# Optimization experiments

Measured on AMD Instinct MI355X. Metric: run time of the kernel, lower is better.

The kernel has to match this reference:

```python
import jax, jax.numpy as jnp
import numpy as np

WS = 7  # window_size


def setup_inputs() -> dict:
    key = jax.random.key(0)
    ks = jax.random.split(key, 4)
    B, C, H, W = 4, 384, 56, 56
    NH = 12
    x = jax.random.normal(ks[0], (B, C, H, W), dtype=jnp.float32)
    # 1x1 conv weights act as per-pixel linear maps over channels
    w_qkv = jax.random.normal(ks[1], (3 * C, C), dtype=jnp.float32) * (C ** -0.5)
    b_qkv = jnp.zeros((3 * C,), dtype=jnp.float32)
    w_proj = jax.random.normal(ks[2], (C, C), dtype=jnp.float32) * (C ** -0.5)
    b_proj = jnp.zeros((C,), dtype=jnp.float32)
    rel_bias = jax.random.normal(ks[3], (NH, WS, WS), dtype=jnp.float32) * 0.02
    return {"x": x, "w_qkv": w_qkv, "b_qkv": b_qkv,
            "w_proj": w_proj, "b_proj": b_proj, "rel_bias": rel_bias}


def reference(x, w_qkv, b_qkv, w_proj, b_proj, rel_bias):
    # Neighborhood attention: each query (i,j) attends to a ws x ws window of
    # keys/values centered at (i,j); borders handled by replication padding
    # (ReplicationPad2d), with a learned relative position bias (nh, ws, ws).
    B, C, H, W = x.shape
    nh, ws, _ = rel_bias.shape
    hd = C // nh
    p = ws // 2
    scale = hd ** -0.5

    # qkv 1x1 conv -> (B, 3, nh, hd, H, W)
    qkv = jnp.einsum('oc,bchw->bohw', w_qkv, x) + b_qkv[None, :, None, None]
    qkv = qkv.reshape(B, 3, nh, hd, H, W)
    q, k, v = qkv[:, 0] * scale, qkv[:, 1], qkv[:, 2]

    pad = ((0, 0), (0, 0), (0, 0), (p, p), (p, p))
    k_pad = jnp.pad(k, pad, mode='edge')  # replication padding
    v_pad = jnp.pad(v, pad, mode='edge')

    # attention logits over the ws*ws window offsets: (B, nh, H, W, K)
    logits = jnp.stack(
        [jnp.einsum('bnchw,bnchw->bnhw', q, k_pad[..., di:di + H, dj:dj + W])
         for di in range(ws) for dj in range(ws)], axis=-1)
    logits = logits + rel_bias.reshape(nh, ws * ws)[None, :, None, None, :]
    attn = jax.nn.softmax(logits, axis=-1)  # (attn_drop is identity in eval)

    # value windows: (B, nh, K, hd, H, W)
    v_win = jnp.stack([v_pad[..., di:di + H, dj:dj + W]
                       for di in range(ws) for dj in range(ws)], axis=2)
    out = jnp.einsum('bnhwk,bnkchw->bnchw', attn, v_win).reshape(B, C, H, W)

    # output projection 1x1 conv (proj_drop is identity in eval)
    out = jnp.einsum('oc,bchw->bohw', w_proj, out) + b_proj[None, :, None, None]
    return out
```

## Files before the change

kernel.cpp:

```cpp
#include <hip/hip_runtime.h>
#include <hip/hip_bf16.h>
#include <hip/hip_fp16.h>

#define S_HW 3136
#define SP   3200
#define IMG_W 56
#define C_DIM 384
#define NH_DIM 12
#define QKV_C 1152

#define TB 16
#define HALO 22
#define NPX 484
#define PLANE_B 3880

typedef float f32x4 __attribute__((ext_vector_type(4)));
typedef float f32x2 __attribute__((ext_vector_type(2)));
typedef short bf16x8 __attribute__((ext_vector_type(8)));
typedef _Float16 f16x2 __attribute__((ext_vector_type(2)));

__device__ __forceinline__ void gld_lds16(const void* g, void* lds) {
    __builtin_amdgcn_global_load_lds(
        (const __attribute__((address_space(1))) void*)g,
        (__attribute__((address_space(3))) void*)lds, 16, 0, 0);
}

__device__ __forceinline__ float u2f(unsigned int u) { return __uint_as_float(u); }
__device__ __forceinline__ unsigned int f2bf_bits(float f) {
    unsigned int u = __float_as_uint(f);
    u += 0x7FFF + ((u >> 16) & 1);
    return u >> 16;
}
__device__ __forceinline__ unsigned int f2h_bits(float f) {
    return (unsigned int)__half_as_ushort(__float2half(f));
}

__global__ __launch_bounds__(256) void convert_w2_kernel(
    const float* __restrict__ a, int na, __hip_bfloat16* __restrict__ oa,
    const float* __restrict__ b, int nb, __hip_bfloat16* __restrict__ ob)
{
    int i = blockIdx.x * 256 + threadIdx.x;
    if (i < na) oa[i] = __float2bfloat16(a[i]);
    else if (i < na + nb) ob[i - na] = __float2bfloat16(b[i - na]);
}

__global__ __launch_bounds__(256) void transpose_convert_kernel(
    const float* __restrict__ x, __hip_bfloat16* __restrict__ xt)
{
    __shared__ float t[32][33];
    const int b = blockIdx.z;
    const int c0 = blockIdx.y * 32, s0 = blockIdx.x * 32;
    const int tid = threadIdx.x;

    const int lc = tid >> 3, ls = (tid & 7) * 4;
    float4 v = *reinterpret_cast<const float4*>(
        &x[((size_t)b * C_DIM + c0 + lc) * S_HW + s0 + ls]);
    t[lc][ls + 0] = v.x; t[lc][ls + 1] = v.y;
    t[lc][ls + 2] = v.z; t[lc][ls + 3] = v.w;
    __syncthreads();

    const int ws = tid >> 3, wc = (tid & 7) * 4;
    uint2 pk;
    pk.x = f2bf_bits(t[wc + 0][ws]) | (f2bf_bits(t[wc + 1][ws]) << 16);
    pk.y = f2bf_bits(t[wc + 2][ws]) | (f2bf_bits(t[wc + 3][ws]) << 16);
    *reinterpret_cast<uint2*>(
        &xt[((size_t)b * SP + s0 + ws) * C_DIM + c0 + wc]) = pk;
}

template <bool TRANS_OUT, int NF, typename OutT>
__global__ __launch_bounds__(256) void gemm_bf16_mfma(
    const __hip_bfloat16* __restrict__ A,
    const __hip_bfloat16* __restrict__ Bt,
    const float* __restrict__ bias,
    OutT* __restrict__ Y,
    int O, int K, float qscale, int qrows)
{
    constexpr int BN = NF * 32;
    __shared__ char smem[8192 + BN * 64];
    char* As = smem;
    char* Bs = smem + 8192;

    const int b   = blockIdx.z;
    const int m0  = blockIdx.y * 128;
    const int n0  = blockIdx.x * BN;
    const int tid = threadIdx.x;
    const int w = tid >> 6, l = tid & 63;
    const int wr = w >> 1, wc = w & 1;

    const int srow = l >> 2;
    const int skk  = (l & 3) * 8;

    const __hip_bfloat16* Bb = Bt + (size_t)b * SP * K;

    f32x4 acc[4][NF];
    #pragma unroll
    for (int i = 0; i < 4; ++i)
        #pragma unroll
        for (int j = 0; j < NF; ++j) {
            f32x4 z = {0.f, 0.f, 0.f, 0.f};
            acc[i][j] = z;
        }

    const int frow = l & 15;
    const int fk   = (l >> 4) * 16;

    for (int k0 = 0; k0 < K; k0 += 32) {
        #pragma unroll
        for (int j = 0; j < 2; ++j) {
            const int chunk = w * 2 + j;
            const int m = chunk * 16 + srow;
            gld_lds16(A + (size_t)(m0 + m) * K + k0 + skk, As + chunk * 1024);
        }
        if (NF == 4) {
            #pragma unroll
            for (int j = 0; j < 2; ++j) {
                const int chunk = w * 2 + j;
                const int m = chunk * 16 + srow;
                gld_lds16(Bb + (size_t)(n0 + m) * K + k0 + skk, Bs + chunk * 1024);
            }
        } else {
            const int m = w * 16 + srow;
            gld_lds16(Bb + (size_t)(n0 + m) * K + k0 + skk, Bs + w * 1024);
        }
        __syncthreads();
        bf16x8 af[4], bfr[NF];
        #pragma unroll
        for (int mi = 0; mi < 4; ++mi)
            af[mi] = *reinterpret_cast<const bf16x8*>(
                As + (wr * 64 + mi * 16 + frow) * 64 + fk);
        #pragma unroll
        for (int ni = 0; ni < NF; ++ni)
            bfr[ni] = *reinterpret_cast<const bf16x8*>(
                Bs + (wc * (NF * 16) + ni * 16 + frow) * 64 + fk);
        #pragma unroll
        for (int mi = 0; mi < 4; ++mi)
            #pragma unroll
            for (int ni = 0; ni < NF; ++ni)
                acc[mi][ni] = __builtin_amdgcn_mfma_f32_16x16x32_bf16(
                    af[mi], bfr[ni], acc[mi][ni], 0, 0, 0);
        __syncthreads();
    }

    const int crow0 = (l >> 4) * 4;
    const int ccol  = l & 15;
    if (TRANS_OUT) {
        __hip_bfloat16* Yb = (__hip_bfloat16*)Y + (size_t)b * SP * O;
        #pragma unroll
        for (int ni = 0; ni < NF; ++ni) {
            const int col = n0 + wc * (NF * 16) + ni * 16 + ccol;
            if (col >= S_HW) continue;
            #pragma unroll
            for (int mi = 0; mi < 4; ++mi) {
                const int row0 = m0 + wr * 64 + mi * 16 + crow0;
                const float sc = (row0 < qrows) ? qscale : 1.f;
                float v0 = (acc[mi][ni][0] + bias[row0 + 0]) * sc;
                float v1 = (acc[mi][ni][1] + bias[row0 + 1]) * sc;
                float v2 = (acc[mi][ni][2] + bias[row0 + 2]) * sc;
                float v3 = (acc[mi][ni][3] + bias[row0 + 3]) * sc;
                uint2 pk;
                pk.x = f2h_bits(v0) | (f2h_bits(v1) << 16);
                pk.y = f2h_bits(v2) | (f2h_bits(v3) << 16);
                *reinterpret_cast<uint2*>(&Yb[(size_t)col * O + row0]) = pk;
            }
        }
    } else {
        float* Yb = (float*)Y + (size_t)b * O * S_HW;
        #pragma unroll
        for (int ni = 0; ni < NF; ++ni) {
            const int col = n0 + wc * (NF * 16) + ni * 16 + ccol;
            if (col >= S_HW) continue;
            #pragma unroll
            for (int mi = 0; mi < 4; ++mi) {
                #pragma unroll
                for (int r = 0; r < 4; ++r) {
                    const int row = m0 + wr * 64 + mi * 16 + crow0 + r;
                    float v = acc[mi][ni][r] + bias[row];
                    if (row < qrows) v *= qscale;
                    Yb[(size_t)row * S_HW + col] = v;
                }
            }
        }
    }
}

__global__ __launch_bounds__(256, 2) void na_attn_kernel(
    const __hip_bfloat16* __restrict__ qkvt, const float* __restrict__ rel_bias,
    __hip_bfloat16* __restrict__ outt)
{
    __shared__ alignas(16) char halo[8 * PLANE_B];

    const int blk  = blockIdx.x;
    const int tile = blk & 15;
    const int bn   = blk >> 4;
    const int nh   = bn % NH_DIM;
    const int b    = bn / NH_DIM;
    const int th0  = (tile >> 2) * TB;
    const int tw0  = (tile & 3) * TB;

    const int tid = threadIdx.x;
    const int ty = tid >> 4, tx = tid & 15;
    const int h = th0 + ty, w = tw0 + tx;
    const bool valid = (h < 56) && (w < 56);
    const int s = h * IMG_W + w;

    const __hip_bfloat16* base = qkvt + (size_t)b * SP * QKV_C;
    const int co = nh * 32;

    #pragma unroll
    for (int i = 0; i < 8; ++i) {
        const int idx = tid + i * 256;
        if (idx < NPX * 4) {
            const int px = idx >> 2, g = idx & 3;
            const int hy = px / HALO, hx = px - hy * HALO;
            const int y = min(max(th0 - 3 + hy, 0), 55);
            const int x = min(max(tw0 - 3 + hx, 0), 55);
            const uint4 v = *reinterpret_cast<const uint4*>(
                base + (size_t)(y * IMG_W + x) * QKV_C + C_DIM + co + g * 8);
            uint2 lo; lo.x = v.x; lo.y = v.y;
            uint2 hi; hi.x = v.z; hi.y = v.w;
            *reinterpret_cast<uint2*>(&halo[(2 * g + 0) * PLANE_B + px * 8]) = lo;
            *reinterpret_cast<uint2*>(&halo[(2 * g + 1) * PLANE_B + px * 8]) = hi;
        }
    }

    unsigned int qreg[16];
    if (valid) {
        const uint4* qp = reinterpret_cast<const uint4*>(base + (size_t)s * QKV_C + co);
        #pragma unroll
        for (int g = 0; g < 4; ++g) {
            uint4 qg = qp[g];
            qreg[4 * g + 0] = qg.x; qreg[4 * g + 1] = qg.y;
            qreg[4 * g + 2] = qg.z; qreg[4 * g + 3] = qg.w;
        }
    }
    __syncthreads();

    float logits[49];
    if (valid) {
        #pragma unroll
        for (int di = 0; di < 7; ++di) {
            #pragma unroll
            for (int dj = 0; dj < 7; ++dj) {
                const int hp = (ty + di) * HALO + (tx + dj);
                const char* hb = halo + hp * 8;
                float acc0 = 0.f, acc1 = 0.f;
                #pragma unroll
                for (int pl = 0; pl < 8; ++pl) {
                    uint2 kk = *reinterpret_cast<const uint2*>(hb + pl * PLANE_B);
#if __has_builtin(__builtin_amdgcn_fdot2)
                    acc0 = __builtin_amdgcn_fdot2(
                        __builtin_bit_cast(f16x2, qreg[2 * pl]),
                        __builtin_bit_cast(f16x2, kk.x), acc0, false);
                    acc1 = __builtin_amdgcn_fdot2(
                        __builtin_bit_cast(f16x2, qreg[2 * pl + 1]),
                        __builtin_bit_cast(f16x2, kk.y), acc1, false);
#else
                    f16x2 qa = __builtin_bit_cast(f16x2, qreg[2 * pl]);
                    f16x2 qb = __builtin_bit_cast(f16x2, qreg[2 * pl + 1]);
                    f16x2 ka = __builtin_bit_cast(f16x2, kk.x);
                    f16x2 kb = __builtin_bit_cast(f16x2, kk.y);
                    acc0 += (float)qa[0] * (float)ka[0] + (float)qa[1] * (float)ka[1];
                    acc1 += (float)qb[0] * (float)kb[0] + (float)qb[1] * (float)kb[1];
#endif
                }
                logits[di * 7 + dj] = acc0 + acc1 + rel_bias[(nh * 7 + di) * 7 + dj];
            }
        }
    }
    __syncthreads();

    #pragma unroll
    for (int i = 0; i < 8; ++i) {
        const int idx = tid + i * 256;
        if (idx < NPX * 4) {
            const int px = idx >> 2, g = idx & 3;
            const int hy = px / HALO, hx = px - hy * HALO;
            const int y = min(max(th0 - 3 + hy, 0), 55);
            const int x = min(max(tw0 - 3 + hx, 0), 55);
            const uint4 v = *reinterpret_cast<const uint4*>(
                base + (size_t)(y * IMG_W + x) * QKV_C + 2 * C_DIM + co + g * 8);
            uint2 lo; lo.x = v.x; lo.y = v.y;
            uint2 hi; hi.x = v.z; hi.y = v.w;
            *reinterpret_cast<uint2*>(&halo[(2 * g + 0) * PLANE_B + px * 8]) = lo;
            *reinterpret_cast<uint2*>(&halo[(2 * g + 1) * PLANE_B + px * 8]) = hi;
        }
    }

    unsigned int ppk[25];
    float inv = 0.f;
    if (valid) {
        float mx = logits[0];
        #pragma unroll
        for (int i = 1; i < 49; ++i) mx = fmaxf(mx, logits[i]);
        float sum = 0.f;
        #pragma unroll
        for (int i = 0; i < 24; ++i) {
            float e0 = __expf(logits[2 * i] - mx);
            float e1 = __expf(logits[2 * i + 1] - mx);
            sum += e0 + e1;
            ppk[i] = f2bf_bits(e0) << 16 | f2bf_bits(e1);
        }
        {
            float e0 = __expf(logits[48] - mx);
            sum += e0;
            ppk[24] = f2bf_bits(e0) << 16;
        }
        inv = 1.f / sum;
    }
    __syncthreads();

    if (valid) {
        float o[32];
        #pragma unroll
        for (int c = 0; c < 32; ++c) o[c] = 0.f;

        #pragma unroll
        for (int n = 0; n < 49; ++n) {
            const unsigned int pu = ppk[n >> 1];
            const float pv = (n & 1) ? u2f(pu << 16) : u2f(pu & 0xFFFF0000u);
            const int di = n / 7, dj = n % 7;
            const int hp = (ty + di) * HALO + (tx + dj);
            const char* hb = halo + hp * 8;
            #pragma unroll
            for (int pl = 0; pl < 8; ++pl) {
                uint2 vv = *reinterpret_cast<const uint2*>(hb + pl * PLANE_B);
                f16x2 va = __builtin_bit_cast(f16x2, vv.x);
                f16x2 vb = __builtin_bit_cast(f16x2, vv.y);
                o[4 * pl + 0] = fmaf((float)va[0], pv, o[4 * pl + 0]);
                o[4 * pl + 1] = fmaf((float)va[1], pv, o[4 * pl + 1]);
                o[4 * pl + 2] = fmaf((float)vb[0], pv, o[4 * pl + 2]);
                o[4 * pl + 3] = fmaf((float)vb[1], pv, o[4 * pl + 3]);
            }
        }

        uint4* dst = reinterpret_cast<uint4*>(outt + ((size_t)b * SP + s) * C_DIM + co);
        #pragma unroll
        for (int g = 0; g < 4; ++g) {
            uint4 pk;
            pk.x = f2bf_bits(o[8 * g + 0] * inv) | (f2bf_bits(o[8 * g + 1] * inv) << 16);
            pk.y = f2bf_bits(o[8 * g + 2] * inv) | (f2bf_bits(o[8 * g + 3] * inv) << 16);
            pk.z = f2bf_bits(o[8 * g + 4] * inv) | (f2bf_bits(o[8 * g + 5] * inv) << 16);
            pk.w = f2bf_bits(o[8 * g + 6] * inv) | (f2bf_bits(o[8 * g + 7] * inv) << 16);
            dst[g] = pk;
        }
    }
}

extern "C" void kernel_launch(void* const* d_in, const int* in_sizes, int n_in,
                              void* d_out, int out_size, void* d_ws, size_t ws_size,
                              hipStream_t stream) {
    const float* x        = (const float*)d_in[0];
    const float* w_qkv    = (const float*)d_in[1];
    const float* b_qkv    = (const float*)d_in[2];
    const float* w_proj   = (const float*)d_in[3];
    const float* b_proj   = (const float*)d_in[4];
    const float* rel_bias = (const float*)d_in[5];
    float* out = (float*)d_out;

    __hip_bfloat16* xt   = (__hip_bfloat16*)d_ws;
    __hip_bfloat16* wq   = xt + (size_t)4 * SP * C_DIM;
    __hip_bfloat16* wp   = wq + (size_t)QKV_C * C_DIM;
    __hip_bfloat16* qkvt = wp + (size_t)C_DIM * C_DIM;
    __hip_bfloat16* att  = qkvt + (size_t)4 * SP * QKV_C;

    const float scale = 0.17677669529663687f;
    const int nwq = QKV_C * C_DIM, nwp = C_DIM * C_DIM;

    convert_w2_kernel<<<dim3((nwq + nwp + 255) / 256), 256, 0, stream>>>(
        w_qkv, nwq, wq, w_proj, nwp, wp);
    transpose_convert_kernel<<<dim3(98, 12, 4), dim3(256), 0, stream>>>(x, xt);

    gemm_bf16_mfma<true, 4, __hip_bfloat16><<<dim3(25, 9, 4), 256, 0, stream>>>(
        wq, xt, b_qkv, qkvt, QKV_C, C_DIM, scale, C_DIM);

    na_attn_kernel<<<dim3(4 * NH_DIM * 16), 256, 0, stream>>>(qkvt, rel_bias, att);

    gemm_bf16_mfma<false, 2, float><<<dim3(50, 3, 4), 256, 0, stream>>>(
        wp, att, b_proj, out, C_DIM, C_DIM, 1.f, 0);
}
```

Before: 97.41 us.

## Split each attention pixel across two threads with DPP pair reduction

The neighborhood-attention kernel now uses 512 threads per block, with two adjacent lanes sharing one pixel and each handling half of the 32 head channels. Partial QK dot products are combined across the lane pair with a DPP swap-and-add. Each lane keeps half as many q registers and output accumulators, and the block has twice as many waves to hide LDS and global latency. In exchange, the softmax over 49 logits is computed redundantly by both lanes, and the launch bound changes from (256,2) to 512.

```diff
diff --git a/kernel.cpp b/kernel.cpp
--- a/kernel.cpp
+++ b/kernel.cpp
@@ -15,7 +15,6 @@
 #define PLANE_B 3880
 
 typedef float f32x4 __attribute__((ext_vector_type(4)));
-typedef float f32x2 __attribute__((ext_vector_type(2)));
 typedef short bf16x8 __attribute__((ext_vector_type(8)));
 typedef _Float16 f16x2 __attribute__((ext_vector_type(2)));
 
@@ -33,6 +32,11 @@
 }
 __device__ __forceinline__ unsigned int f2h_bits(float f) {
     return (unsigned int)__half_as_ushort(__float2half(f));
+}
+
+__device__ __forceinline__ float pair_sum(float v) {
+    int o = __builtin_amdgcn_update_dpp(0, __float_as_int(v), 0xB1, 0xF, 0xF, true);
+    return v + __uint_as_float((unsigned int)o);
 }
 
 __global__ __launch_bounds__(256) void convert_w2_kernel(
@@ -183,7 +187,7 @@
     }
 }
 
-__global__ __launch_bounds__(256, 2) void na_attn_kernel(
+__global__ __launch_bounds__(512) void na_attn_kernel(
     const __hip_bfloat16* __restrict__ qkvt, const float* __restrict__ rel_bias,
     __hip_bfloat16* __restrict__ outt)
 {
@@ -197,41 +201,42 @@
     const int th0  = (tile >> 2) * TB;
     const int tw0  = (tile & 3) * TB;
 
-    const int tid = threadIdx.x;
-    const int ty = tid >> 4, tx = tid & 15;
+    const int tid  = threadIdx.x;
+    const int px   = tid >> 1;
+    const int half = tid & 1;
+    const int ty = px >> 4, tx = px & 15;
     const int h = th0 + ty, w = tw0 + tx;
     const bool valid = (h < 56) && (w < 56);
     const int s = h * IMG_W + w;
 
     const __hip_bfloat16* base = qkvt + (size_t)b * SP * QKV_C;
     const int co = nh * 32;
+    const int pl0 = 4 * half;
 
     #pragma unroll
-    for (int i = 0; i < 8; ++i) {
-        const int idx = tid + i * 256;
+    for (int i = 0; i < 4; ++i) {
+        const int idx = tid + i * 512;
         if (idx < NPX * 4) {
-            const int px = idx >> 2, g = idx & 3;
-            const int hy = px / HALO, hx = px - hy * HALO;
+            const int p = idx >> 2, g = idx & 3;
+            const int hy = p / HALO, hx = p - hy * HALO;
             const int y = min(max(th0 - 3 + hy, 0), 55);
             const int x = min(max(tw0 - 3 + hx, 0), 55);
             const uint4 v = *reinterpret_cast<const uint4*>(
                 base + (size_t)(y * IMG_W + x) * QKV_C + C_DIM + co + g * 8);
             uint2 lo; lo.x = v.x; lo.y = v.y;
             uint2 hi; hi.x = v.z; hi.y = v.w;
-            *reinterpret_cast<uint2*>(&halo[(2 * g + 0) * PLANE_B + px * 8]) = lo;
-            *reinterpret_cast<uint2*>(&halo[(2 * g + 1) * PLANE_B + px * 8]) = hi;
-        }
-    }
-
-    unsigned int qreg[16];
+            *reinterpret_cast<uint2*>(&halo[(2 * g + 0) * PLANE_B + p * 8]) = lo;
+            *reinterpret_cast<uint2*>(&halo[(2 * g + 1) * PLANE_B + p * 8]) = hi;
+        }
+    }
+
+    unsigned int qreg[8];
     if (valid) {
-        const uint4* qp = reinterpret_cast<const uint4*>(base + (size_t)s * QKV_C + co);
-        #pragma unroll
-        for (int g = 0; g < 4; ++g) {
-            uint4 qg = qp[g];
-            qreg[4 * g + 0] = qg.x; qreg[4 * g + 1] = qg.y;
-            qreg[4 * g + 2] = qg.z; qreg[4 * g + 3] = qg.w;
-        }
+        const uint4* qp = reinterpret_cast<const uint4*>(
+            base + (size_t)s * QKV_C + co + 16 * half);
+        uint4 q0 = qp[0], q1 = qp[1];
+        qreg[0] = q0.x; qreg[1] = q0.y; qreg[2] = q0.z; qreg[3] = q0.w;
+        qreg[4] = q1.x; qreg[5] = q1.y; qreg[6] = q1.z; qreg[7] = q1.w;
     }
     __syncthreads();
 
@@ -245,8 +250,9 @@
                 const char* hb = halo + hp * 8;
                 float acc0 = 0.f, acc1 = 0.f;
                 #pragma unroll
-                for (int pl = 0; pl < 8; ++pl) {
-                    uint2 kk = *reinterpret_cast<const uint2*>(hb + pl * PLANE_B);
+                for (int pl = 0; pl < 4; ++pl) {
+                    uint2 kk = *reinterpret_cast<const uint2*>(
+                        hb + (pl0 + pl) * PLANE_B);
 #if __has_builtin(__builtin_amdgcn_fdot2)
                     acc0 = __builtin_amdgcn_fdot2(
                         __builtin_bit_cast(f16x2, qreg[2 * pl]),
@@ -263,26 +269,27 @@
                     acc1 += (float)qb[0] * (float)kb[0] + (float)qb[1] * (float)kb[1];
 #endif
                 }
-                logits[di * 7 + dj] = acc0 + acc1 + rel_bias[(nh * 7 + di) * 7 + dj];
+                logits[di * 7 + dj] =
+                    pair_sum(acc0 + acc1) + rel_bias[(nh * 7 + di) * 7 + dj];
             }
         }
     }
     __syncthreads();
 
     #pragma unroll
-    for (int i = 0; i < 8; ++i) {
-        const int idx = tid + i * 256;
+    for (int i = 0; i < 4; ++i) {
+        const int idx = tid + i * 512;
         if (idx < NPX * 4) {
-            const int px = idx >> 2, g = idx & 3;
-            const int hy = px / HALO, hx = px - hy * HALO;
+            const int p = idx >> 2, g = idx & 3;
+            const int hy = p / HALO, hx = p - hy * HALO;
             const int y = min(max(th0 - 3 + hy, 0), 55);
             const int x = min(max(tw0 - 3 + hx, 0), 55);
             const uint4 v = *reinterpret_cast<const uint4*>(
                 base + (size_t)(y * IMG_W + x) * QKV_C + 2 * C_DIM + co + g * 8);
             uint2 lo; lo.x = v.x; lo.y = v.y;
             uint2 hi; hi.x = v.z; hi.y = v.w;
-            *reinterpret_cast<uint2*>(&halo[(2 * g + 0) * PLANE_B + px * 8]) = lo;
-            *reinterpret_cast<uint2*>(&halo[(2 * g + 1) * PLANE_B + px * 8]) = hi;
+            *reinterpret_cast<uint2*>(&halo[(2 * g + 0) * PLANE_B + p * 8]) = lo;
+            *reinterpret_cast<uint2*>(&halo[(2 * g + 1) * PLANE_B + p * 8]) = hi;
         }
     }
 
@@ -310,9 +317,9 @@
     __syncthreads();
 
     if (valid) {
-        float o[32];
-        #pragma unroll
-        for (int c = 0; c < 32; ++c) o[c] = 0.f;
+        float o[16];
+        #pragma unroll
+        for (int c = 0; c < 16; ++c) o[c] = 0.f;
 
         #pragma unroll
         for (int n = 0; n < 49; ++n) {
@@ -322,8 +329,9 @@
             const int hp = (ty + di) * HALO + (tx + dj);
             const char* hb = halo + hp * 8;
             #pragma unroll
-            for (int pl = 0; pl < 8; ++pl) {
-                uint2 vv = *reinterpret_cast<const uint2*>(hb + pl * PLANE_B);
+            for (int pl = 0; pl < 4; ++pl) {
+                uint2 vv = *reinterpret_cast<const uint2*>(
+                    hb + (pl0 + pl) * PLANE_B);
                 f16x2 va = __builtin_bit_cast(f16x2, vv.x);
                 f16x2 vb = __builtin_bit_cast(f16x2, vv.y);
                 o[4 * pl + 0] = fmaf((float)va[0], pv, o[4 * pl + 0]);
@@ -333,9 +341,10 @@
             }
         }
 
-        uint4* dst = reinterpret_cast<uint4*>(outt + ((size_t)b * SP + s) * C_DIM + co);
-        #pragma unroll
-        for (int g = 0; g < 4; ++g) {
+        uint4* dst = reinterpret_cast<uint4*>(
+            outt + ((size_t)b * SP + s) * C_DIM + co + 16 * half);
+        #pragma unroll
+        for (int g = 0; g < 2; ++g) {
             uint4 pk;
             pk.x = f2bf_bits(o[8 * g + 0] * inv) | (f2bf_bits(o[8 * g + 1] * inv) << 16);
             pk.y = f2bf_bits(o[8 * g + 2] * inv) | (f2bf_bits(o[8 * g + 3] * inv) << 16);
@@ -373,7 +382,7 @@
     gemm_bf16_mfma<true, 4, __hip_bfloat16><<<dim3(25, 9, 4), 256, 0, stream>>>(
         wq, xt, b_qkv, qkvt, QKV_C, C_DIM, scale, C_DIM);
 
-    na_attn_kernel<<<dim3(4 * NH_DIM * 16), 256, 0, stream>>>(qkvt, rel_bias, att);
+    na_attn_kernel<<<dim3(4 * NH_DIM * 16), 512, 0, stream>>>(qkvt, rel_bias, att);
 
     gemm_bf16_mfma<false, 2, float><<<dim3(50, 3, 4), 256, 0, stream>>>(
         wp, att, b_proj, out, C_DIM, C_DIM, 1.f, 0);
```

Result: slower. 104.3 us (+7.1%).
